# Kernel optimization log

Measured on AMD Instinct MI355X. Metric: run time of the kernel, lower is better.

The kernel has to match this reference:

```python
import jax, jax.numpy as jnp
import numpy as np

T, B, D, H = 8192, 4, 1024, 16  # seq_len, batch, d_model, n_heads


def setup_inputs() -> dict:
    key = jax.random.key(0)
    k1, k2, k3 = jax.random.split(key, 3)
    s = 1.0 / np.sqrt(D).astype(np.float32)
    return {
        "query": jax.random.normal(k1, (T, B, D), jnp.float32),
        "Wqkv": jax.random.normal(k2, (3 * D, D), jnp.float32) * s,
        "bqkv": jnp.zeros((3 * D,), jnp.float32),
        "Wout": jax.random.normal(k3, (D, D), jnp.float32) * s,
        "bout": jnp.zeros((D,), jnp.float32),
    }


def reference(query, Wqkv, bqkv, Wout, bout):
    Tl, Bs, Dm = query.shape
    hd = Dm // H
    # fused qkv projection: [T,B,3D]
    qkv = query @ Wqkv.T + bqkv
    q, k, v = jnp.split(qkv, 3, axis=-1)

    def heads(x):
        # torch: view(T, B*H, hd).transpose(0,1).view(B,H,T,hd)
        return x.reshape(Tl, Bs, H, hd).transpose(1, 2, 0, 3)  # [B,H,T,hd]

    qh, kh, vh = heads(q), heads(k), heads(v)

    # corrcoef over head_dim axis, T is the sample axis: X,Y are [B,H,hd,T]
    X = jnp.swapaxes(qh, -1, -2)
    Y = jnp.swapaxes(kh, -1, -2)
    Xc = X - X.mean(-1, keepdims=True)
    Yc = Y - Y.mean(-1, keepdims=True)
    c = jnp.einsum('bhiT,bhjT->bhij', Xc, Yc)          # [B,H,hd,hd] covariance
    sx = (Xc * Xc).sum(-1, keepdims=True)              # [B,H,hd,1]
    sy = (Yc * Yc).sum(-1)[..., None, :]               # [B,H,1,hd]
    corr = jnp.clip(c / jnp.sqrt(sx * sy), 0.0, 1.0)
    corr = jax.nn.softmax(corr, axis=-2)               # softmax over rows (dim=-2)

    # weighted sum: v @ corr  -> [B,H,T,hd]
    attn = jnp.einsum('bhtd,bhde->bhte', vh, corr)
    # permute(2,0,1,3).view(T*B, D) then out_proj then view(T,B,D)
    out = attn.transpose(2, 0, 1, 3).reshape(Tl * Bs, Dm) @ Wout.T + bout
    return out.reshape(Tl, Bs, Dm)
```

## Files before the change

### kernel.cpp

```cpp
#include <hip/hip_runtime.h>
#include <stdint.h>


typedef unsigned short u16;
typedef __attribute__((ext_vector_type(8))) short bf16x8;
typedef __attribute__((ext_vector_type(8))) u16  u16x8;
typedef __attribute__((ext_vector_type(4))) float f32x4;

#define AS1 __attribute__((address_space(1)))
#define AS3 __attribute__((address_space(3)))

__device__ __forceinline__ u16 f2b(float f) {
  union { float f; uint32_t u; } x; x.f = f;
  const uint32_t u = x.u;
  return (u16)((u + 0x7FFFu + ((u >> 16) & 1u)) >> 16);
}
__device__ __forceinline__ void g2l16(const void* g, void* l) {
  __builtin_amdgcn_global_load_lds((const AS1 uint32_t*)g, (AS3 uint32_t*)l, 16, 0, 0);
}
__device__ __forceinline__ bf16x8 lds_read16(uint32_t addr) {
  bf16x8 r;
  asm volatile("ds_read_b128 %0, %1" : "=&v"(r) : "v"(addr) : "memory");
  return r;
}

__global__ __launch_bounds__(256) void cvt_all(
    const float* __restrict__ q, const float* __restrict__ w1, const float* __restrict__ w2,
    u16* __restrict__ qb, u16* __restrict__ w1b, u16* __restrict__ w2b)
{
  int i = blockIdx.x * 256 + threadIdx.x;
  if (i >= 4718592) return;
  const float* s; u16* d; int ofs;
  if (i < 4194304)      { s = q;  d = qb;  ofs = i; }
  else if (i < 4587520) { s = w1; d = w1b; ofs = i - 4194304; }
  else                  { s = w2; d = w2b; ofs = i - 4587520; }
  const float4 a = *(const float4*)(s + (size_t)ofs * 8);
  const float4 b = *(const float4*)(s + (size_t)ofs * 8 + 4);
  u16x8 o;
  o[0] = f2b(a.x); o[1] = f2b(a.y); o[2] = f2b(a.z); o[3] = f2b(a.w);
  o[4] = f2b(b.x); o[5] = f2b(b.y); o[6] = f2b(b.z); o[7] = f2b(b.w);
  *(u16x8*)(d + (size_t)ofs * 8) = o;
}

#define BARX() do { asm volatile("" ::: "memory");                    \
                    __builtin_amdgcn_s_barrier();                     \
                    asm volatile("" ::: "memory"); } while (0)

#define WAITDS(N) do {                                                \
    asm volatile("s_waitcnt lgkmcnt(" #N ")" ::: "memory");           \
    __builtin_amdgcn_sched_barrier(0); } while (0)

#define KEEP4(X) asm volatile("" :: "v"(X[0]), "v"(X[1]), "v"(X[2]), "v"(X[3]))

#define MROW(AF, BF, AB, M_)                                          \
  _Pragma("unroll") for (int n_ = 0; n_ < 4; ++n_)                    \
    acc[(AB) + (M_)][n_] = __builtin_amdgcn_mfma_f32_16x16x32_bf16(   \
        AF[M_], BF[n_], acc[(AB) + (M_)][n_], 0, 0, 0);

#define PH_EVEN(BUF, KH, Q, AF, BF, AFO, BFO) do {                    \
    const uint32_t qo_ = ((BUF) * 2 + (KH)) * 16384u;                 \
    BF[0] = lds_read16(boffB[0] + qo_);                               \
    BF[1] = lds_read16(boffB[1] + qo_);                               \
    BF[2] = lds_read16(boffB[2] + qo_);                               \
    BF[3] = lds_read16(boffB[3] + qo_);                               \
    AF[0] = lds_read16(aoffB[0][0] + qo_);                            \
    AF[1] = lds_read16(aoffB[0][1] + qo_);                            \
    AF[2] = lds_read16(aoffB[0][2] + qo_);                            \
    AF[3] = lds_read16(aoffB[0][3] + qo_);                            \
    issue_half(Q);                                                    \
    BARX();                                                           \
    WAITDS(3); __builtin_amdgcn_s_setprio(1); MROW(AF, BF, 0, 0);     \
    WAITDS(2); MROW(AF, BF, 0, 1);                                    \
    WAITDS(1); MROW(AF, BF, 0, 2);                                    \
    WAITDS(0); MROW(AF, BF, 0, 3); __builtin_amdgcn_s_setprio(0);     \
    KEEP4(AFO); KEEP4(BFO);                                           \
    BARX();                                                           \
  } while (0)

#define PH_ODD(BUF, KH, Q, AF, BF, AFO, BFO, TAILWAIT) do {           \
    const uint32_t qo_ = ((BUF) * 2 + (KH)) * 16384u;                 \
    AF[0] = lds_read16(aoffB[1][0] + qo_);                            \
    AF[1] = lds_read16(aoffB[1][1] + qo_);                            \
    AF[2] = lds_read16(aoffB[1][2] + qo_);                            \
    AF[3] = lds_read16(aoffB[1][3] + qo_);                            \
    issue_half(Q);                                                    \
    BARX();                                                           \
    WAITDS(3); __builtin_amdgcn_s_setprio(1); MROW(AF, BF, 4, 0);     \
    WAITDS(2); MROW(AF, BF, 4, 1);                                    \
    WAITDS(1); MROW(AF, BF, 4, 2);                                    \
    WAITDS(0); MROW(AF, BF, 4, 3); __builtin_amdgcn_s_setprio(0);     \
    KEEP4(AFO); KEEP4(BFO);                                           \
    TAILWAIT;                                                         \
    BARX();                                                           \
  } while (0)

#define GTILE(T, TAILWAIT) do {                                       \
    const int buf_ = (T) & 1;                                         \
    PH_EVEN(buf_, 0, 4 * (T) + 6, afA, bfA, afB, bfB);                \
    PH_ODD (buf_, 0, 4 * (T) + 7, afB, bfA, afA, bfB, (void)0);       \
    PH_EVEN(buf_, 1, 4 * (T) + 8, afA, bfB, afB, bfA);                \
    PH_ODD (buf_, 1, 4 * (T) + 9, afB, bfB, afA, bfA, TAILWAIT);      \
  } while (0)

template <int MODE>
__global__ __launch_bounds__(512, 2) void gemm8p(
    const u16* __restrict__ A, const u16* __restrict__ B,
    const float* __restrict__ bias, void* __restrict__ OutP)
{
  __shared__ __align__(16) u16 As[2][2][8192];
  __shared__ __align__(16) u16 Bs[2][2][8192];
  const int tid = threadIdx.x;
  int bn, bm, batch;
  if (MODE == 0) { bn = blockIdx.x & 31; bm = (blockIdx.x >> 5) & 7; batch = blockIdx.x >> 8; }
  else           { bn = blockIdx.x & 3;  bm = blockIdx.x >> 2;       batch = 0; }
  const int m0 = bm * 256, n0 = bn * 256;
  const int lane = tid & 63, wave = tid >> 6;
  const int wr = wave >> 2, wc = wave & 3;
  const int laneN = lane & 15, laneQ = lane >> 4;

  const u16* Abase = A + (size_t)m0 * 1024;
  const size_t bPitch = (MODE == 0) ? 4096 : 1024;
  const u16* Bbase = (MODE == 0) ? (B + (size_t)batch * 1024 + (size_t)n0 * 4096)
                                 : (B + (size_t)n0 * 1024);

  const uint32_t AsB = (uint32_t)(uintptr_t)(const AS3 u16*)&As[0][0][0];
  const uint32_t BsB = (uint32_t)(uintptr_t)(const AS3 u16*)&Bs[0][0][0];
  uint32_t aoffB[2][4], boffB[4];
#pragma unroll
  for (int mh = 0; mh < 2; ++mh)
#pragma unroll
    for (int m = 0; m < 4; ++m) {
      const int row = wr * 128 + mh * 64 + m * 16 + laneN;
      const int sl = laneQ ^ ((row >> 1) & 3);
      aoffB[mh][m] = AsB + (uint32_t)(row * 64 + sl * 16);
    }
#pragma unroll
  for (int n = 0; n < 4; ++n) {
    const int row = wc * 64 + n * 16 + laneN;
    const int sl = laneQ ^ ((row >> 1) & 3);
    boffB[n] = BsB + (uint32_t)(row * 64 + sl * 16);
  }

  const int sr = tid >> 2, sl = tid & 3;
  const int qg = sl ^ ((sr >> 1) & 3);
  const size_t aofs0 = (size_t)sr * 1024 + qg * 8;
  const size_t aofs1 = aofs0 + (size_t)128 * 1024;
  const size_t bofs0 = (size_t)sr * bPitch + qg * 8;
  const size_t bofs1 = bofs0 + (size_t)128 * bPitch;

  auto issue_half = [&](int q) {
    if (q >= 64) return;
    const int tq = q >> 2, ty = q & 3;
    const int bufq = tq & 1, kh = ty >> 1;
    const int kofs = tq * 64 + kh * 32;
    if ((ty & 1) == 0) {
      u16* l = &As[bufq][kh][tid * 8];
      g2l16(Abase + aofs0 + kofs, l);
      g2l16(Abase + aofs1 + kofs, l + 4096);
    } else {
      u16* l = &Bs[bufq][kh][tid * 8];
      g2l16(Bbase + bofs0 + kofs, l);
      g2l16(Bbase + bofs1 + kofs, l + 4096);
    }
  };

  f32x4 acc[8][4] = {};
  bf16x8 afA[4] = {}, afB[4] = {}, bfA[4] = {}, bfB[4] = {};

#pragma unroll
  for (int q = 0; q < 6; ++q) issue_half(q);
  asm volatile("s_waitcnt vmcnt(4)" ::: "memory");
  __builtin_amdgcn_s_barrier();
  asm volatile("" ::: "memory");

#pragma unroll 2
  for (int t = 0; t < 14; ++t)
    GTILE(t, asm volatile("s_waitcnt vmcnt(4)" ::: "memory"));
  GTILE(14, asm volatile("s_waitcnt vmcnt(0)" ::: "memory"));
  GTILE(15, (void)0);

  if (MODE == 0) {
#pragma unroll
    for (int m = 0; m < 8; ++m) {
#pragma unroll
      for (int r = 0; r < 4; ++r) {
        const int f = m0 + wr * 128 + m * 16 + laneQ * 4 + r;
        const float bv = bias[f];
        const int seg = f >> 10, h = (f & 1023) >> 6, d = f & 63;
        u16* base = (u16*)OutP + (size_t)seg * 33554432 +
                    ((size_t)((batch * 16 + h) * 64 + d)) * 8192;
#pragma unroll
        for (int n = 0; n < 4; ++n) {
          const int t = n0 + wc * 64 + n * 16 + laneN;
          base[t] = f2b(acc[m][n][r] + bv);
        }
      }
    }
  } else {
#pragma unroll
    for (int m = 0; m < 8; ++m) {
#pragma unroll
      for (int n = 0; n < 4; ++n) {
        const int col = n0 + wc * 64 + n * 16 + laneN;
        const float bv = bias[col];
#pragma unroll
        for (int r = 0; r < 4; ++r) {
          const int row = m0 + wr * 128 + m * 16 + laneQ * 4 + r;
          const float v = acc[m][n][r] + bv;
          if (MODE == 1) ((u16*)OutP)[(size_t)row * 1024 + col] = f2b(v);
          else           ((float*)OutP)[(size_t)row * 1024 + col] = v;
        }
      }
    }
  }
}

#undef GTILE
#undef PH_ODD
#undef PH_EVEN
#undef MROW
#undef KEEP4
#undef WAITDS
#undef BARX

__global__ __launch_bounds__(256) void stats_k(
    const u16* __restrict__ qT, const u16* __restrict__ kT,
    float* __restrict__ Spart, float* __restrict__ Mpart)
{
  __shared__ __align__(16) u16 smem[2 * 4 * 64 * 64];
  __shared__ float margLDS[4 * 256];
  u16* Qs = smem;
  u16* Ks = smem + 16384;
  const int tid = threadIdx.x;
  const int bh = blockIdx.x & 63;
  const int chunk = blockIdx.x >> 6;
  const int t0 = chunk * 1024;
  const int lane = tid & 63, wave = tid >> 6;
  const int laneN = lane & 15, laneQ = lane >> 4;

  const u16* qp = qT + (size_t)bh * 524288;
  const u16* kp = kT + (size_t)bh * 524288;

  f32x4 accS[4][4] = {};
  f32x4 accQQ[4] = {}, accKK[4] = {}, accQ1[4] = {}, accK1[4] = {};
  bf16x8 ones;
#pragma unroll
  for (int j = 0; j < 8; ++j) ones[j] = (short)0x3F80;

  for (int rd = 0; rd < 4; ++rd) {
    __syncthreads();
#pragma unroll
    for (int i = 0; i < 8; ++i) {
      const int c = tid + i * 256;
      const int tile = c >> 9, cw = c & 511;
      const int d = cw >> 3, slot = cw & 7;
      const int kb = slot ^ (d & 7);
      const size_t gofs = (size_t)d * 8192 + (t0 + rd * 256 + tile * 64 + kb * 8);
      g2l16(qp + gofs, &Qs[c * 8]);
      g2l16(kp + gofs, &Ks[c * 8]);
    }
    __syncthreads();
    const u16* qt = &Qs[wave * 4096];
    const u16* kt2 = &Ks[wave * 4096];
#pragma unroll
    for (int ks2 = 0; ks2 < 2; ++ks2) {
      bf16x8 qf[4], kf[4];
#pragma unroll
      for (int i = 0; i < 4; ++i) {
        const int d = i * 16 + laneN;
        const int kq = (ks2 * 4 + laneQ) ^ (d & 7);
        qf[i] = *(const bf16x8*)&qt[d * 64 + kq * 8];
        kf[i] = *(const bf16x8*)&kt2[d * 64 + kq * 8];
      }
#pragma unroll
      for (int i = 0; i < 4; ++i) {
#pragma unroll
        for (int j = 0; j < 4; ++j)
          accS[i][j] = __builtin_amdgcn_mfma_f32_16x16x32_bf16(qf[i], kf[j], accS[i][j], 0, 0, 0);
        accQQ[i] = __builtin_amdgcn_mfma_f32_16x16x32_bf16(qf[i], qf[i], accQQ[i], 0, 0, 0);
        accKK[i] = __builtin_amdgcn_mfma_f32_16x16x32_bf16(kf[i], kf[i], accKK[i], 0, 0, 0);
        accQ1[i] = __builtin_amdgcn_mfma_f32_16x16x32_bf16(qf[i], ones, accQ1[i], 0, 0, 0);
        accK1[i] = __builtin_amdgcn_mfma_f32_16x16x32_bf16(kf[i], ones, accK1[i], 0, 0, 0);
      }
    }
  }

  __syncthreads();
  float* red = (float*)smem;
#pragma unroll
  for (int i = 0; i < 4; ++i)
#pragma unroll
    for (int j = 0; j < 4; ++j)
#pragma unroll
      for (int r = 0; r < 4; ++r) {
        const int d = i * 16 + laneQ * 4 + r, e = j * 16 + laneN;
        red[wave * 4096 + d * 64 + e] = accS[i][j][r];
      }
#pragma unroll
  for (int i = 0; i < 4; ++i) {
    if (laneN == 0) {
#pragma unroll
      for (int r = 0; r < 4; ++r) {
        const int d = i * 16 + laneQ * 4 + r;
        margLDS[wave * 256 + 0 * 64 + d] = accQ1[i][r];
        margLDS[wave * 256 + 2 * 64 + d] = accK1[i][r];
      }
    }
    if ((laneN >> 2) == laneQ) {
      const int r = laneN & 3;
      const int d = i * 16 + laneN;
      margLDS[wave * 256 + 1 * 64 + d] = accQQ[i][r];
      margLDS[wave * 256 + 3 * 64 + d] = accKK[i][r];
    }
  }
  __syncthreads();
  float* Sp = Spart + ((size_t)chunk * 64 + bh) * 4096;
  for (int c = tid; c < 4096; c += 256)
    Sp[c] = red[c] + red[4096 + c] + red[8192 + c] + red[12288 + c];
  float* Mp = Mpart + ((size_t)chunk * 64 + bh) * 256;
  Mp[tid] = margLDS[tid] + margLDS[256 + tid] + margLDS[512 + tid] + margLDS[768 + tid];
}

__global__ __launch_bounds__(64) void finalize_k(
    const float* __restrict__ Spart, const float* __restrict__ Mpart,
    u16* __restrict__ corrT)
{
  __shared__ float Ss[4096];
  __shared__ float sqs[64], sxs[64];
  const int bh = blockIdx.x;
  const int e = threadIdx.x;
  for (int idx = e; idx < 4096; idx += 64) {
    float s = 0.f;
#pragma unroll
    for (int c = 0; c < 8; ++c) s += Spart[((size_t)c * 64 + bh) * 4096 + idx];
    Ss[idx] = s;
  }
  float m[4];
#pragma unroll
  for (int p = 0; p < 4; ++p) {
    float s = 0.f;
#pragma unroll
    for (int c = 0; c < 8; ++c) s += Mpart[((size_t)c * 64 + bh) * 256 + p * 64 + e];
    m[p] = s;
  }
  const float invT = 1.0f / 8192.0f;
  const float sy = m[3] - m[2] * m[2] * invT;
  const float ske = m[2];
  sqs[e] = m[0];
  sxs[e] = m[1] - m[0] * m[0] * invT;
  __syncthreads();
  float mx = 0.0f;
  for (int d = 0; d < 64; ++d) {
    const float c = Ss[d * 64 + e] - sqs[d] * ske * invT;
    float r = c / sqrtf(sxs[d] * sy);
    r = fminf(fmaxf(r, 0.0f), 1.0f);
    Ss[d * 64 + e] = r;
    mx = fmaxf(mx, r);
  }
  float sum = 0.f;
  for (int d = 0; d < 64; ++d) {
    const float ev = expf(Ss[d * 64 + e] - mx);
    Ss[d * 64 + e] = ev;
    sum += ev;
  }
  const float inv = 1.0f / sum;
  for (int d = 0; d < 64; ++d)
    corrT[(size_t)bh * 4096 + e * 64 + d] = f2b(Ss[d * 64 + e] * inv);
}

__global__ __launch_bounds__(256) void attn_k(
    const u16* __restrict__ vb, const u16* __restrict__ corrT,
    u16* __restrict__ attnb)
{
  __shared__ __align__(16) u16 Vs[256 * 64];
  __shared__ __align__(16) u16 Cs[64 * 64];
  const int tid = threadIdx.x;
  const int bh = blockIdx.x & 63;
  const int tt0 = (blockIdx.x >> 6) * 256;
  const int b = bh >> 4, h = bh & 15;
  const int lane = tid & 63, wave = tid >> 6;
  const int laneN = lane & 15, laneQ = lane >> 4;

  {
#pragma unroll
    for (int i = 0; i < 8; ++i) {
      const int c = tid + i * 256;
      const int row = c >> 3, slot = c & 7;
      const int kb = slot ^ (row & 7);
      const u16* g = vb + (size_t)((tt0 + row) * 4 + b) * 1024 + h * 64 + kb * 8;
      g2l16(g, &Vs[c * 8]);
    }
#pragma unroll
    for (int i = 0; i < 2; ++i) {
      const int c = tid + i * 256;
      const int row = c >> 3, slot = c & 7;
      const int kb = slot ^ (row & 7);
      g2l16(corrT + (size_t)bh * 4096 + row * 64 + kb * 8, &Cs[c * 8]);
    }
  }
  __syncthreads();

  const int wt = wave * 64;
  f32x4 acc[4][4] = {};
#pragma unroll
  for (int ks2 = 0; ks2 < 2; ++ks2) {
    bf16x8 af[4], bf[4];
#pragma unroll
    for (int i = 0; i < 4; ++i) {
      const int row = wt + i * 16 + laneN;
      const int kq = (ks2 * 4 + laneQ) ^ (row & 7);
      af[i] = *(const bf16x8*)&Vs[row * 64 + kq * 8];
    }
#pragma unroll
    for (int j = 0; j < 4; ++j) {
      const int row = j * 16 + laneN;
      const int kq = (ks2 * 4 + laneQ) ^ (row & 7);
      bf[j] = *(const bf16x8*)&Cs[row * 64 + kq * 8];
    }
#pragma unroll
    for (int i = 0; i < 4; ++i)
#pragma unroll
      for (int j = 0; j < 4; ++j)
        acc[i][j] = __builtin_amdgcn_mfma_f32_16x16x32_bf16(af[i], bf[j], acc[i][j], 0, 0, 0);
  }
#pragma unroll
  for (int i = 0; i < 4; ++i)
#pragma unroll
    for (int j = 0; j < 4; ++j)
#pragma unroll
      for (int r = 0; r < 4; ++r) {
        const int t = tt0 + wt + i * 16 + laneQ * 4 + r;
        const int e = j * 16 + laneN;
        attnb[(size_t)(t * 4 + b) * 1024 + h * 64 + e] = f2b(acc[i][j][r]);
      }
}

extern "C" void kernel_launch(void* const* d_in, const int* in_sizes, int n_in,
                              void* d_out, int out_size, void* d_ws, size_t ws_size,
                              hipStream_t stream)
{
  const float* query = (const float*)d_in[0];
  const float* Wqkv  = (const float*)d_in[1];
  const float* bqkv  = (const float*)d_in[2];
  const float* Wout  = (const float*)d_in[3];
  const float* bout  = (const float*)d_in[4];
  char* ws = (char*)d_ws;

  u16*   qkT    = (u16*)(ws);
  u16*   kT     = (u16*)(ws + 67108864);
  u16*   vb     = (u16*)(ws + 134217728);
  u16*   queryb = (u16*)(ws + 201326592);
  float* Spart  = (float*)(ws + 201326592);
  float* Mpart  = (float*)(ws + 209715200);
  u16*   corrT  = (u16*)(ws + 210239488);
  u16*   Wqkvb  = (u16*)(ws + 268435456);
  u16*   Woutb  = (u16*)(ws + 274726912);

  cvt_all<<<dim3(18432), dim3(256), 0, stream>>>(query, Wqkv, Wout, queryb, Wqkvb, Woutb);

  gemm8p<0><<<dim3(1024), dim3(512), 0, stream>>>(Wqkvb, queryb, bqkv, qkT);
  gemm8p<1><<<dim3(512), dim3(512), 0, stream>>>(queryb, Wqkvb + (size_t)2048 * 1024,
                                                 bqkv + 2048, vb);
  stats_k<<<dim3(512), dim3(256), 0, stream>>>(qkT, kT, Spart, Mpart);
  finalize_k<<<dim3(64), dim3(64), 0, stream>>>(Spart, Mpart, corrT);
  attn_k<<<dim3(2048), dim3(256), 0, stream>>>(vb, corrT, qkT);
  gemm8p<2><<<dim3(512), dim3(512), 0, stream>>>(qkT, Woutb, bout, d_out);
}
```

Before: 639.3 us.

## Restructure GEMM main loop to fewer barriers per K-tile with deeper LDS prefetch

The bf16 MFMA GEMM inner loop is rescheduled. Each K-tile used to run as four phases, each with two workgroup barriers. Now each tile runs as one block with two barriers. All fragment reads for both K-halves are issued up front with finer lgkmcnt waits, and the global-to-LDS prefetches for the next tiles are placed around the single mid-tile barrier. The aim is to cut barrier stalls and keep more LDS reads in flight alongside the MFMAs. The cost is higher register pressure and a more delicate buffer-reuse ordering that depends on the waitcnt placement.

```diff
diff --git a/kernel.cpp b/kernel.cpp
--- a/kernel.cpp
+++ b/kernel.cpp
@@ -50,56 +50,61 @@
     asm volatile("s_waitcnt lgkmcnt(" #N ")" ::: "memory");           \
     __builtin_amdgcn_sched_barrier(0); } while (0)
 
-#define KEEP4(X) asm volatile("" :: "v"(X[0]), "v"(X[1]), "v"(X[2]), "v"(X[3]))
-
 #define MROW(AF, BF, AB, M_)                                          \
   _Pragma("unroll") for (int n_ = 0; n_ < 4; ++n_)                    \
     acc[(AB) + (M_)][n_] = __builtin_amdgcn_mfma_f32_16x16x32_bf16(   \
         AF[M_], BF[n_], acc[(AB) + (M_)][n_], 0, 0, 0);
 
-#define PH_EVEN(BUF, KH, Q, AF, BF, AFO, BFO) do {                    \
-    const uint32_t qo_ = ((BUF) * 2 + (KH)) * 16384u;                 \
-    BF[0] = lds_read16(boffB[0] + qo_);                               \
-    BF[1] = lds_read16(boffB[1] + qo_);                               \
-    BF[2] = lds_read16(boffB[2] + qo_);                               \
-    BF[3] = lds_read16(boffB[3] + qo_);                               \
-    AF[0] = lds_read16(aoffB[0][0] + qo_);                            \
-    AF[1] = lds_read16(aoffB[0][1] + qo_);                            \
-    AF[2] = lds_read16(aoffB[0][2] + qo_);                            \
-    AF[3] = lds_read16(aoffB[0][3] + qo_);                            \
-    issue_half(Q);                                                    \
-    BARX();                                                           \
-    WAITDS(3); __builtin_amdgcn_s_setprio(1); MROW(AF, BF, 0, 0);     \
-    WAITDS(2); MROW(AF, BF, 0, 1);                                    \
-    WAITDS(1); MROW(AF, BF, 0, 2);                                    \
-    WAITDS(0); MROW(AF, BF, 0, 3); __builtin_amdgcn_s_setprio(0);     \
-    KEEP4(AFO); KEEP4(BFO);                                           \
-    BARX();                                                           \
-  } while (0)
-
-#define PH_ODD(BUF, KH, Q, AF, BF, AFO, BFO, TAILWAIT) do {           \
-    const uint32_t qo_ = ((BUF) * 2 + (KH)) * 16384u;                 \
-    AF[0] = lds_read16(aoffB[1][0] + qo_);                            \
-    AF[1] = lds_read16(aoffB[1][1] + qo_);                            \
-    AF[2] = lds_read16(aoffB[1][2] + qo_);                            \
-    AF[3] = lds_read16(aoffB[1][3] + qo_);                            \
-    issue_half(Q);                                                    \
-    BARX();                                                           \
-    WAITDS(3); __builtin_amdgcn_s_setprio(1); MROW(AF, BF, 4, 0);     \
-    WAITDS(2); MROW(AF, BF, 4, 1);                                    \
-    WAITDS(1); MROW(AF, BF, 4, 2);                                    \
-    WAITDS(0); MROW(AF, BF, 4, 3); __builtin_amdgcn_s_setprio(0);     \
-    KEEP4(AFO); KEEP4(BFO);                                           \
+#define GTILE(T, TAILWAIT) do {                                       \
+    const uint32_t q0_ = (uint32_t)((((T) & 1) * 2 + 0) * 16384);     \
+    const uint32_t q1_ = (uint32_t)((((T) & 1) * 2 + 1) * 16384);     \
+                             \
+    bfA[0] = lds_read16(boffB[0] + q0_);                              \
+    bfA[1] = lds_read16(boffB[1] + q0_);                              \
+    bfA[2] = lds_read16(boffB[2] + q0_);                              \
+    bfA[3] = lds_read16(boffB[3] + q0_);                              \
+    afA[0] = lds_read16(aoffB[0][0] + q0_);                           \
+    afA[1] = lds_read16(aoffB[0][1] + q0_);                           \
+    afA[2] = lds_read16(aoffB[0][2] + q0_);                           \
+    afA[3] = lds_read16(aoffB[0][3] + q0_);                           \
+                                       \
+    afB[0] = lds_read16(aoffB[1][0] + q0_);                           \
+    afB[1] = lds_read16(aoffB[1][1] + q0_);                           \
+    afB[2] = lds_read16(aoffB[1][2] + q0_);                           \
+    afB[3] = lds_read16(aoffB[1][3] + q0_);                           \
+    issue_half((T) + 1, 2); issue_half((T) + 1, 3);                   \
+    WAITDS(4);                              \
+    __builtin_amdgcn_s_setprio(1);                                    \
+    MROW(afA, bfA, 0, 0); MROW(afA, bfA, 0, 1);                       \
+    MROW(afA, bfA, 0, 2); MROW(afA, bfA, 0, 3);                       \
+                  \
+    bfB[0] = lds_read16(boffB[0] + q1_);                              \
+    bfB[1] = lds_read16(boffB[1] + q1_);                              \
+    bfB[2] = lds_read16(boffB[2] + q1_);                              \
+    bfB[3] = lds_read16(boffB[3] + q1_);                              \
+    afA[0] = lds_read16(aoffB[0][0] + q1_);                           \
+    afA[1] = lds_read16(aoffB[0][1] + q1_);                           \
+    afA[2] = lds_read16(aoffB[0][2] + q1_);                           \
+    afA[3] = lds_read16(aoffB[0][3] + q1_);                           \
+    WAITDS(8);   \
+    BARX();              \
+    issue_half((T) + 2, 0); issue_half((T) + 2, 1);                   \
+    MROW(afB, bfA, 4, 0); MROW(afB, bfA, 4, 1);                       \
+    MROW(afB, bfA, 4, 2); MROW(afB, bfA, 4, 3);                       \
+                            \
+    afB[0] = lds_read16(aoffB[1][0] + q1_);                           \
+    afB[1] = lds_read16(aoffB[1][1] + q1_);                           \
+    afB[2] = lds_read16(aoffB[1][2] + q1_);                           \
+    afB[3] = lds_read16(aoffB[1][3] + q1_);                           \
+    WAITDS(4);                                           \
+    MROW(afA, bfB, 0, 0); MROW(afA, bfB, 0, 1);                       \
+    MROW(afA, bfB, 0, 2); MROW(afA, bfB, 0, 3);                       \
+    WAITDS(0);                                           \
+    MROW(afB, bfB, 4, 0); MROW(afB, bfB, 4, 1);                       \
+    MROW(afB, bfB, 4, 2); MROW(afB, bfB, 4, 3);                       \
+    __builtin_amdgcn_s_setprio(0);                                    \
     TAILWAIT;                                                         \
     BARX();                                                           \
-  } while (0)
-
-#define GTILE(T, TAILWAIT) do {                                       \
-    const int buf_ = (T) & 1;                                         \
-    PH_EVEN(buf_, 0, 4 * (T) + 6, afA, bfA, afB, bfB);                \
-    PH_ODD (buf_, 0, 4 * (T) + 7, afB, bfA, afA, bfB, (void)0);       \
-    PH_EVEN(buf_, 1, 4 * (T) + 8, afA, bfB, afB, bfA);                \
-    PH_ODD (buf_, 1, 4 * (T) + 9, afB, bfB, afA, bfA, TAILWAIT);      \
   } while (0)
 
 template <int MODE>
@@ -148,12 +153,12 @@
   const size_t bofs0 = (size_t)sr * bPitch + qg * 8;
   const size_t bofs1 = bofs0 + (size_t)128 * bPitch;
 
-  auto issue_half = [&](int q) {
-    if (q >= 64) return;
-    const int tq = q >> 2, ty = q & 3;
-    const int bufq = tq & 1, kh = ty >> 1;
-    const int kofs = tq * 64 + kh * 32;
-    if ((ty & 1) == 0) {
+  auto issue_half = [&](int tile, int half) {
+    if (tile > 15) return;
+    const int kh = half >> 1;
+    const int kofs = tile * 64 + kh * 32;
+    const int bufq = tile & 1;
+    if ((half & 1) == 0) {
       u16* l = &As[bufq][kh][tid * 8];
       g2l16(Abase + aofs0 + kofs, l);
       g2l16(Abase + aofs1 + kofs, l + 4096);
@@ -165,10 +170,10 @@
   };
 
   f32x4 acc[8][4] = {};
-  bf16x8 afA[4] = {}, afB[4] = {}, bfA[4] = {}, bfB[4] = {};
-
-#pragma unroll
-  for (int q = 0; q < 6; ++q) issue_half(q);
+  bf16x8 afA[4], afB[4], bfA[4], bfB[4];
+
+  issue_half(0, 0); issue_half(0, 1); issue_half(0, 2); issue_half(0, 3);
+  issue_half(1, 0); issue_half(1, 1);
   asm volatile("s_waitcnt vmcnt(4)" ::: "memory");
   __builtin_amdgcn_s_barrier();
   asm volatile("" ::: "memory");
@@ -216,10 +221,7 @@
 }
 
 #undef GTILE
-#undef PH_ODD
-#undef PH_EVEN
 #undef MROW
-#undef KEEP4
 #undef WAITDS
 #undef BARX
 
```

Measured after the change: 763.3 us. 1.19x slower.
